# Kernel optimization log

Measured on AMD Instinct MI355X. Metric: run time of the kernel, lower is better.

## Reference

```python
import jax, jax.numpy as jnp
import numpy as np

N, E, G = 50000, 500000, 64
DIN, ED, H1, H2, HD, OUT = 128, 32, 256, 128, 64, 8


def setup_inputs() -> dict:
    key = jax.random.key(0)
    ks = jax.random.split(key, 20)
    g = lambda i, shape: (jax.random.normal(ks[i], shape, jnp.float32) * 0.05)
    return dict(
        node_attr=jax.random.normal(ks[0], (N, DIN), jnp.float32),
        edge_attr=jax.random.normal(ks[1], (E, ED), jnp.float32),
        edge_src=jax.random.randint(ks[2], (E,), 0, N, jnp.int32),
        edge_dst=jax.random.randint(ks[3], (E,), 0, N, jnp.int32),
        batch=jnp.sort(jax.random.randint(ks[4], (N,), 0, G, jnp.int32)),
        Wl1=g(5, (DIN, H1)), bl1=jnp.zeros((H1,), jnp.float32),
        Wr1=g(6, (DIN, H1)), br1=jnp.zeros((H1,), jnp.float32),
        We1=g(7, (ED, H1)), att1=g(8, (H1,)), b1=jnp.zeros((H1,), jnp.float32),
        Wl2=g(9, (H1, H2)), bl2=jnp.zeros((H2,), jnp.float32),
        Wr2=g(10, (H1, H2)), br2=jnp.zeros((H2,), jnp.float32),
        We2=g(11, (ED, H2)), att2=g(12, (H2,)), b2=jnp.zeros((H2,), jnp.float32),
        Wd1=g(13, (H2, HD)), bd1=jnp.zeros((HD,), jnp.float32),
        bn_gamma=jnp.ones((HD,), jnp.float32), bn_beta=jnp.zeros((HD,), jnp.float32),
        bn_mean=jnp.zeros((HD,), jnp.float32), bn_var=jnp.ones((HD,), jnp.float32),
        Wd2=g(14, (HD, OUT)), bd2=jnp.zeros((OUT,), jnp.float32),
    )


def gatv2(x, src, dst, eattr, Wl, bl, Wr, br, We, att, bias, n):
    # PyG GATv2Conv, heads=1: add self-loops (fill_value='mean' for edge_attr)
    ones = jnp.ones((eattr.shape[0],), x.dtype)
    deg = jax.ops.segment_sum(ones, dst, n)
    loop_attr = jax.ops.segment_sum(eattr, dst, n) / jnp.maximum(deg, 1.0)[:, None]
    loop = jnp.arange(n, dtype=src.dtype)
    src_ = jnp.concatenate([src, loop])
    dst_ = jnp.concatenate([dst, loop])
    eattr_ = jnp.concatenate([eattr, loop_attr], axis=0)
    xl = x @ Wl + bl  # [n, C] source transform (lin_l)
    xr = x @ Wr + br  # [n, C] dest transform (lin_r)
    # edge-wise GATv2 score: a^T LeakyReLU(xl_j + xr_i + We e_ij)
    e = jax.nn.leaky_relu(xl[src_] + xr[dst_] + eattr_ @ We, 0.2) @ att  # [E+n]
    m = jax.ops.segment_max(e, dst_, n)
    w = jnp.exp(e - m[dst_])
    denom = jax.ops.segment_sum(w, dst_, n)
    alpha = w / denom[dst_]
    return jax.ops.segment_sum(alpha[:, None] * xl[src_], dst_, n) + bias


def reference(node_attr, edge_attr, edge_src, edge_dst, batch,
              Wl1, bl1, Wr1, br1, We1, att1, b1,
              Wl2, bl2, Wr2, br2, We2, att2, b2,
              Wd1, bd1, bn_gamma, bn_beta, bn_mean, bn_var, Wd2, bd2):
    x = jax.nn.relu(gatv2(node_attr, edge_src, edge_dst, edge_attr,
                          Wl1, bl1, Wr1, br1, We1, att1, b1, N))
    x = jax.nn.relu(gatv2(x, edge_src, edge_dst, edge_attr,
                          Wl2, bl2, Wr2, br2, We2, att2, b2, N))
    # global mean pool over graphs
    cnt = jax.ops.segment_sum(jnp.ones((N,), x.dtype), batch, G)
    x = jax.ops.segment_sum(x, batch, G) / jnp.maximum(cnt, 1.0)[:, None]
    x = x @ Wd1 + bd1
    # BatchNorm1d in eval mode (running stats); dropout is identity in eval
    x = (x - bn_mean) / jnp.sqrt(bn_var + 1e-5) * bn_gamma + bn_beta
    x = jax.nn.leaky_relu(x, 0.1)
    return x @ Wd2 + bd2
```

## Files before the change

### kernel.cpp

```cpp
#include <hip/hip_runtime.h>
#include <cstdint>
#include <cstddef>
#include <cmath>

constexpr int Nn = 50000;
constexpr int Ne = 500000;
constexpr int Gg = 64;
constexpr int DIN = 128, ED = 32, H1 = 256, H2 = 128, HD = 64, NOUT = 8;

typedef __attribute__((ext_vector_type(8))) short bf16x8;
typedef __attribute__((ext_vector_type(4))) float f32x4;

__device__ __forceinline__ unsigned short f2bf(float x) {
    unsigned u = __float_as_uint(x);
    u += 0x7FFFu + ((u >> 16) & 1u);
    return (unsigned short)(u >> 16);
}
__device__ __forceinline__ float bf2f(unsigned short h) {
    return __uint_as_float(((unsigned)h) << 16);
}

__global__ void count_deg_kernel(const int* __restrict__ dst, int* __restrict__ deg) {
    int e = blockIdx.x * 256 + threadIdx.x;
    if (e < Ne) atomicAdd(&deg[dst[e]], 1);
}

__global__ __launch_bounds__(1024) void scan_kernel(const int* __restrict__ deg,
                                                    int* __restrict__ row_start) {
    __shared__ int part[1024];
    int t = threadIdx.x;
    const int chunk = (Nn + 1023) / 1024;
    int lo = t * chunk;
    int hi = min(lo + chunk, Nn);
    int s = 0;
    for (int i = lo; i < hi; i++) s += deg[i];
    part[t] = s;
    __syncthreads();
    for (int off = 1; off < 1024; off <<= 1) {
        int add = (t >= off) ? part[t - off] : 0;
        __syncthreads();
        part[t] += add;
        __syncthreads();
    }
    int base = (t == 0) ? 0 : part[t - 1];
    for (int i = lo; i < hi; i++) { row_start[i] = base; base += deg[i]; }
    if (t == 0) row_start[Nn] = Ne;
}

__global__ void scatter_kernel(const int* __restrict__ dst, const int* __restrict__ row_start,
                               int* __restrict__ cursor, int* __restrict__ perm) {
    int e = blockIdx.x * 256 + threadIdx.x;
    if (e < Ne) {
        int d = dst[e];
        int p = atomicAdd(&cursor[d], 1);
        perm[row_start[d] + p] = e;
    }
}

__global__ void build_sd_kernel(const int* __restrict__ perm, const int* __restrict__ src,
                                const int* __restrict__ dst,
                                int* __restrict__ srcv, int* __restrict__ dstv) {
    int j = blockIdx.x * 256 + threadIdx.x;
    if (j < Ne) {
        int e = perm[j];
        srcv[j] = src[e];
        dstv[j] = dst[e];
    }
}

__global__ void loop_attr_kernel(const int* __restrict__ row_start, const int* __restrict__ perm,
                                 const float* __restrict__ eattr, float* __restrict__ loop_attr) {
    int tid = blockIdx.x * 256 + threadIdx.x;
    if (tid >= Nn * 8) return;
    int i = tid >> 3, q = (tid & 7) << 2;
    int r0 = row_start[i], r1 = row_start[i + 1];
    float4 s = make_float4(0.f, 0.f, 0.f, 0.f);
    for (int j = r0; j < r1; j++) {
        int e = perm[j];
        float4 v = *(const float4*)(eattr + (size_t)e * ED + q);
        s.x += v.x; s.y += v.y; s.z += v.z; s.w += v.w;
    }
    float inv = 1.0f / fmaxf((float)(r1 - r0), 1.0f);
    *(float4*)(loop_attr + (size_t)i * ED + q) =
        make_float4(s.x * inv, s.y * inv, s.z * inv, s.w * inv);
}

__global__ void cvt_wt6_kernel(
    const float* __restrict__ We1, unsigned short* __restrict__ w1hi, unsigned short* __restrict__ w1lo,
    const float* __restrict__ We2, unsigned short* __restrict__ w2hi, unsigned short* __restrict__ w2lo,
    const float* __restrict__ Wl1, unsigned short* __restrict__ wl1hi, unsigned short* __restrict__ wl1lo,
    const float* __restrict__ Wr1, unsigned short* __restrict__ wr1hi, unsigned short* __restrict__ wr1lo,
    const float* __restrict__ Wl2, unsigned short* __restrict__ wl2hi, unsigned short* __restrict__ wl2lo,
    const float* __restrict__ Wr2, unsigned short* __restrict__ wr2hi, unsigned short* __restrict__ wr2lo) {
    const float* W; unsigned short *hi, *lo; int K, N;
    switch (blockIdx.y) {
        case 0: W = We1; hi = w1hi;  lo = w1lo;  K = ED;  N = H1; break;
        case 1: W = We2; hi = w2hi;  lo = w2lo;  K = ED;  N = H2; break;
        case 2: W = Wl1; hi = wl1hi; lo = wl1lo; K = DIN; N = H1; break;
        case 3: W = Wr1; hi = wr1hi; lo = wr1lo; K = DIN; N = H1; break;
        case 4: W = Wl2; hi = wl2hi; lo = wl2lo; K = H1;  N = H2; break;
        default: W = Wr2; hi = wr2hi; lo = wr2lo; K = H1;  N = H2; break;
    }
    int t = blockIdx.x * 256 + threadIdx.x;
    if (t >= K * N) return;
    int col = t / K, k = t % K;
    float x = W[(size_t)k * N + col];
    unsigned short h = f2bf(x);
    hi[t] = h;
    lo[t] = f2bf(x - bf2f(h));
}

template <int K, int N>
__global__ __launch_bounds__(256) void gemm_mfma_kernel(
    int M, const float* __restrict__ A,
    const unsigned short* __restrict__ wt0hi, const unsigned short* __restrict__ wt0lo,
    const float* __restrict__ bias0, float* __restrict__ C0,
    const unsigned short* __restrict__ wt1hi, const unsigned short* __restrict__ wt1lo,
    const float* __restrict__ bias1, float* __restrict__ C1) {
    const unsigned short* wthi = blockIdx.z ? wt1hi : wt0hi;
    const unsigned short* wtlo = blockIdx.z ? wt1lo : wt0lo;
    const float* bias = blockIdx.z ? bias1 : bias0;
    float* Cc = blockIdx.z ? C1 : C0;
    constexpr int KC = (K > 128) ? 128 : K;
    constexpr int P = KC + 8;
    constexpr int NT = N / 64;
    constexpr int CH = KC / 4;
    __shared__ unsigned short Ah[64 * P], Al[64 * P];
    const int tid = threadIdx.x;
    const int m0 = blockIdx.y * 64;

    const int wv = tid >> 6, lane = tid & 63;
    const int g = lane >> 4, li = lane & 15;
    const int nb = wv * (N / 4);

    f32x4 acc[4][NT];
#pragma unroll
    for (int n = 0; n < NT; n++) {
        float bc = bias[nb + n * 16 + li];
#pragma unroll
        for (int m = 0; m < 4; m++) {
            acc[m][n][0] = bc; acc[m][n][1] = bc; acc[m][n][2] = bc; acc[m][n][3] = bc;
        }
    }

    for (int kc = 0; kc < K; kc += KC) {
        for (int t = tid; t < 64 * CH; t += 256) {
            int row = t / CH, c = t % CH;
            int gr = min(m0 + row, M - 1);
            float4 v = *(const float4*)(A + (size_t)gr * K + kc + c * 4);
            unsigned short h0 = f2bf(v.x), h1 = f2bf(v.y), h2 = f2bf(v.z), h3 = f2bf(v.w);
            unsigned short l0 = f2bf(v.x - bf2f(h0)), l1 = f2bf(v.y - bf2f(h1));
            unsigned short l2 = f2bf(v.z - bf2f(h2)), l3 = f2bf(v.w - bf2f(h3));
            *(ushort4*)&Ah[row * P + c * 4] = make_ushort4(h0, h1, h2, h3);
            *(ushort4*)&Al[row * P + c * 4] = make_ushort4(l0, l1, l2, l3);
        }
        __syncthreads();

#pragma unroll
        for (int kt = 0; kt < KC / 32; kt++) {
            bf16x8 afh[4], afl[4], bfh[NT], bfl[NT];
#pragma unroll
            for (int m = 0; m < 4; m++) {
                afh[m] = *(const bf16x8*)&Ah[(m * 16 + li) * P + kt * 32 + g * 8];
                afl[m] = *(const bf16x8*)&Al[(m * 16 + li) * P + kt * 32 + g * 8];
            }
#pragma unroll
            for (int n = 0; n < NT; n++) {
                int col = nb + n * 16 + li;
                bfh[n] = *(const bf16x8*)(wthi + (size_t)col * K + kc + kt * 32 + g * 8);
                bfl[n] = *(const bf16x8*)(wtlo + (size_t)col * K + kc + kt * 32 + g * 8);
            }
#pragma unroll
            for (int m = 0; m < 4; m++)
#pragma unroll
                for (int n = 0; n < NT; n++) {
                    acc[m][n] = __builtin_amdgcn_mfma_f32_16x16x32_bf16(afh[m], bfh[n], acc[m][n], 0, 0, 0);
                    acc[m][n] = __builtin_amdgcn_mfma_f32_16x16x32_bf16(afh[m], bfl[n], acc[m][n], 0, 0, 0);
                    acc[m][n] = __builtin_amdgcn_mfma_f32_16x16x32_bf16(afl[m], bfh[n], acc[m][n], 0, 0, 0);
                }
        }
        __syncthreads();
    }

#pragma unroll
    for (int m = 0; m < 4; m++)
#pragma unroll
        for (int n = 0; n < NT; n++) {
            int col = nb + n * 16 + li;
#pragma unroll
            for (int r = 0; r < 4; r++) {
                int node = m0 + m * 16 + g * 4 + r;
                if (node < M) Cc[(size_t)node * N + col] = acc[m][n][r];
            }
        }
}

template <int C>
__global__ __launch_bounds__((C / 64) * 64) void score_mfma4_kernel(
    int ecount, int eblocks, const int* __restrict__ perm,
    const int* __restrict__ srcv, const int* __restrict__ dstv,
    const float* __restrict__ eattr, float* __restrict__ esc,
    int ncount, const float* __restrict__ lattr, float* __restrict__ nsc,
    const float* __restrict__ xl, const float* __restrict__ xr,
    const unsigned short* __restrict__ wthi, const unsigned short* __restrict__ wtlo,
    const float* __restrict__ att) {
    constexpr int WPB = C / 64;
    constexpr int NTHR = WPB * 64;
    __shared__ unsigned short Ah[64 * 40], Al[64 * 40];
    __shared__ float pw[WPB][64];
    const int tid = threadIdx.x;
    const bool selfp = (int)blockIdx.x >= eblocks;
    const int bid = selfp ? ((int)blockIdx.x - eblocks) : (int)blockIdx.x;
    const int count = selfp ? ncount : ecount;
    const float* attr = selfp ? lattr : eattr;
    float* sc_out = selfp ? nsc : esc;
    const int j0 = bid * 64;

    for (int t = tid; t < 64 * 8; t += NTHR) {
        int row = t >> 3, c = t & 7;
        int j = min(j0 + row, count - 1);
        int e = selfp ? j : perm[j];
        float4 v = *(const float4*)(attr + (size_t)e * ED + c * 4);
        unsigned short h0 = f2bf(v.x), h1 = f2bf(v.y), h2 = f2bf(v.z), h3 = f2bf(v.w);
        unsigned short l0 = f2bf(v.x - bf2f(h0)), l1 = f2bf(v.y - bf2f(h1));
        unsigned short l2 = f2bf(v.z - bf2f(h2)), l3 = f2bf(v.w - bf2f(h3));
        *(ushort4*)&Ah[row * 40 + c * 4] = make_ushort4(h0, h1, h2, h3);
        *(ushort4*)&Al[row * 40 + c * 4] = make_ushort4(l0, l1, l2, l3);
    }
    __syncthreads();

    const int wv = tid >> 6, lane = tid & 63;
    const int g = lane >> 4, li = lane & 15;
    const int cb = wv * 64 + g * 4;

    bf16x8 af_h[4], af_l[4];
#pragma unroll
    for (int m = 0; m < 4; m++) {
        int col = wv * 64 + m * 16 + li;
        af_h[m] = *(const bf16x8*)(wthi + (size_t)col * ED + g * 8);
        af_l[m] = *(const bf16x8*)(wtlo + (size_t)col * ED + g * 8);
    }
    float4 attv[4];
#pragma unroll
    for (int m = 0; m < 4; m++) attv[m] = *(const float4*)(att + cb + m * 16);

    int s0, d0, s1, d1, s2, d2, s3, d3;
    {
        int j;
        j = min(j0 + 0 * 16 + li, count - 1);
        s0 = selfp ? j : srcv[j]; d0 = selfp ? j : dstv[j];
        j = min(j0 + 1 * 16 + li, count - 1);
        s1 = selfp ? j : srcv[j]; d1 = selfp ? j : dstv[j];
        j = min(j0 + 2 * 16 + li, count - 1);
        s2 = selfp ? j : srcv[j]; d2 = selfp ? j : dstv[j];
        j = min(j0 + 3 * 16 + li, count - 1);
        s3 = selfp ? j : srcv[j]; d3 = selfp ? j : dstv[j];
    }

    auto pf = [&](int n, int sE, int dE, bf16x8& bh, bf16x8& bl,
                  float4 (&xlv)[4], float4 (&xrv)[4]) {
        bh = *(const bf16x8*)&Ah[(n * 16 + li) * 40 + g * 8];
        bl = *(const bf16x8*)&Al[(n * 16 + li) * 40 + g * 8];
        const float* pl = xl + (size_t)sE * C + cb;
        const float* pr = xr + (size_t)dE * C + cb;
#pragma unroll
        for (int m = 0; m < 4; m++) {
            xlv[m] = *(const float4*)(pl + m * 16);
            xrv[m] = *(const float4*)(pr + m * 16);
        }
    };
    auto comp = [&](int n, bf16x8 bh, bf16x8 bl,
                    const float4 (&xlv)[4], const float4 (&xrv)[4]) {
        f32x4 acc[4];
#pragma unroll
        for (int m = 0; m < 4; m++) {
            acc[m][0] = xlv[m].x + xrv[m].x; acc[m][1] = xlv[m].y + xrv[m].y;
            acc[m][2] = xlv[m].z + xrv[m].z; acc[m][3] = xlv[m].w + xrv[m].w;
        }
#pragma unroll
        for (int m = 0; m < 4; m++) {
            acc[m] = __builtin_amdgcn_mfma_f32_16x16x32_bf16(af_h[m], bh, acc[m], 0, 0, 0);
            acc[m] = __builtin_amdgcn_mfma_f32_16x16x32_bf16(af_h[m], bl, acc[m], 0, 0, 0);
            acc[m] = __builtin_amdgcn_mfma_f32_16x16x32_bf16(af_l[m], bh, acc[m], 0, 0, 0);
        }
        float s = 0.f;
#pragma unroll
        for (int m = 0; m < 4; m++) {
            const float av[4] = {attv[m].x, attv[m].y, attv[m].z, attv[m].w};
#pragma unroll
            for (int r = 0; r < 4; r++) {
                float z = acc[m][r];
                z = z > 0.f ? z : 0.2f * z;
                s = fmaf(z, av[r], s);
            }
        }
        s += __shfl_xor(s, 16);
        s += __shfl_xor(s, 32);
        if (lane < 16) pw[wv][n * 16 + li] = s;
    };

    bf16x8 bhA, blA, bhB, blB;
    float4 xlA[4], xrA[4], xlB[4], xrB[4];
    pf(0, s0, d0, bhA, blA, xlA, xrA);
    pf(1, s1, d1, bhB, blB, xlB, xrB);
    comp(0, bhA, blA, xlA, xrA);
    pf(2, s2, d2, bhA, blA, xlA, xrA);
    comp(1, bhB, blB, xlB, xrB);
    pf(3, s3, d3, bhB, blB, xlB, xrB);
    comp(2, bhA, blA, xlA, xrA);
    comp(3, bhB, blB, xlB, xrB);

    __syncthreads();
    if (tid < 64) {
        float s = pw[0][tid];
#pragma unroll
        for (int w = 1; w < WPB; w++) s += pw[w][tid];
        int j = j0 + tid;
        if (j < count) sc_out[j] = s;
    }
}

template <int C>
__global__ __launch_bounds__(256) void aggregate2_kernel(
    const int* __restrict__ row_start, const int* __restrict__ srcv,
    const float* __restrict__ scores, const float* __restrict__ sscore,
    const float* __restrict__ xl, const float* __restrict__ bias,
    float* __restrict__ xout) {
    constexpr int VP = C / 64;
    const int wave = threadIdx.x >> 6, lane = threadIdx.x & 63;
    const int i = blockIdx.x * 4 + wave;
    if (i >= Nn) return;
    const int r0 = row_start[i], r1 = row_start[i + 1];

    float mx = sscore[i];
    for (int j = r0 + lane; j < r1; j += 64) mx = fmaxf(mx, scores[j]);
#pragma unroll
    for (int off = 32; off >= 1; off >>= 1) mx = fmaxf(mx, __shfl_xor(mx, off));

    float l = 0.f;
    float acc[VP];
#pragma unroll
    for (int j = 0; j < VP; j++) acc[j] = 0.f;

    float wA[4], xA[4][VP];
    auto load_batch = [&](int j0, float* w, float (*x)[VP]) {
#pragma unroll
        for (int q = 0; q < 4; q++) {
            int j = min(j0 + q, r1 - 1);
            w[q] = scores[j];
            const float* p = xl + (size_t)srcv[j] * C + lane * VP;
            if constexpr (VP == 4) {
                float4 v = *(const float4*)p;
                x[q][0] = v.x; x[q][1] = v.y; x[q][2] = v.z; x[q][3] = v.w;
            } else {
                float2 v = *(const float2*)p;
                x[q][0] = v.x; x[q][1] = v.y;
            }
        }
    };
    if (r0 < r1) load_batch(r0, wA, xA);

    for (int j0 = r0; j0 < r1; j0 += 4) {
        float wB[4], xB[4][VP];
        if (j0 + 4 < r1) load_batch(j0 + 4, wB, xB);
        const int nb = min(4, r1 - j0);
        for (int q = 0; q < nb; q++) {
            float w = __expf(wA[q] - mx);
            l += w;
#pragma unroll
            for (int j = 0; j < VP; j++) acc[j] = fmaf(w, xA[q][j], acc[j]);
        }
        if (j0 + 4 < r1) {
#pragma unroll
            for (int q = 0; q < 4; q++) {
                wA[q] = wB[q];
#pragma unroll
                for (int j = 0; j < VP; j++) xA[q][j] = xB[q][j];
            }
        }
    }

    {
        float w = __expf(sscore[i] - mx);
        l += w;
        const float* p = xl + (size_t)i * C + lane * VP;
        if constexpr (VP == 4) {
            float4 v = *(const float4*)p;
            acc[0] = fmaf(w, v.x, acc[0]); acc[1] = fmaf(w, v.y, acc[1]);
            acc[2] = fmaf(w, v.z, acc[2]); acc[3] = fmaf(w, v.w, acc[3]);
        } else {
            float2 v = *(const float2*)p;
            acc[0] = fmaf(w, v.x, acc[0]); acc[1] = fmaf(w, v.y, acc[1]);
        }
    }

    float invl = 1.0f / l;
    float* xo = xout + (size_t)i * C + lane * VP;
    if constexpr (VP == 4) {
        float4 bv = *(const float4*)(bias + lane * 4);
        float4 o;
        o.x = fmaxf(fmaf(acc[0], invl, bv.x), 0.f);
        o.y = fmaxf(fmaf(acc[1], invl, bv.y), 0.f);
        o.z = fmaxf(fmaf(acc[2], invl, bv.z), 0.f);
        o.w = fmaxf(fmaf(acc[3], invl, bv.w), 0.f);
        *(float4*)xo = o;
    } else {
        float2 bv = *(const float2*)(bias + lane * 2);
        float2 o;
        o.x = fmaxf(fmaf(acc[0], invl, bv.x), 0.f);
        o.y = fmaxf(fmaf(acc[1], invl, bv.y), 0.f);
        *(float2*)xo = o;
    }
}

__global__ __launch_bounds__(128) void pool2_kernel(const float* __restrict__ x2,
                                                    const int* __restrict__ batch,
                                                    float* __restrict__ pooled,
                                                    float* __restrict__ cnt) {
    const int c = threadIdx.x;
    const int chunk = (Nn + gridDim.x - 1) / gridDim.x;
    int lo = blockIdx.x * chunk;
    int hi = min(lo + chunk, Nn);
    if (lo >= hi) return;
    int gcur = batch[lo];
    float acc = 0.f, ncnt = 0.f;
    for (int i = lo; i < hi; i++) {
        int g = batch[i];
        if (g != gcur) {
            atomicAdd(&pooled[gcur * H2 + c], acc);
            if (c == 0) atomicAdd(&cnt[gcur], ncnt);
            acc = 0.f; ncnt = 0.f; gcur = g;
        }
        acc += x2[(size_t)i * H2 + c];
        ncnt += 1.f;
    }
    atomicAdd(&pooled[gcur * H2 + c], acc);
    if (c == 0) atomicAdd(&cnt[gcur], ncnt);
}

__global__ __launch_bounds__(64) void head_kernel(
    const float* __restrict__ pooled, const float* __restrict__ cnt,
    const float* __restrict__ Wd1, const float* __restrict__ bd1,
    const float* __restrict__ gamma, const float* __restrict__ beta,
    const float* __restrict__ mean, const float* __restrict__ var,
    const float* __restrict__ Wd2, const float* __restrict__ bd2,
    float* __restrict__ out) {
    __shared__ float xm[H2];
    __shared__ float h[HD];
    int g = blockIdx.x, t = threadIdx.x;
    float c = fmaxf(cnt[g], 1.0f);
    for (int i = t; i < H2; i += 64) xm[i] = pooled[g * H2 + i] / c;
    __syncthreads();
    float a = bd1[t];
    for (int k = 0; k < H2; k++) a = fmaf(xm[k], Wd1[k * HD + t], a);
    a = (a - mean[t]) / sqrtf(var[t] + 1e-5f) * gamma[t] + beta[t];
    a = a > 0.f ? a : 0.1f * a;
    h[t] = a;
    __syncthreads();
    if (t < NOUT) {
        float o = bd2[t];
        for (int k = 0; k < HD; k++) o = fmaf(h[k], Wd2[k * NOUT + t], o);
        out[g * NOUT + t] = o;
    }
}

extern "C" void kernel_launch(void* const* d_in, const int* in_sizes, int n_in,
                              void* d_out, int out_size, void* d_ws, size_t ws_size,
                              hipStream_t stream) {
    const float* node_attr = (const float*)d_in[0];
    const float* edge_attr = (const float*)d_in[1];
    const int* edge_src = (const int*)d_in[2];
    const int* edge_dst = (const int*)d_in[3];
    const int* batch = (const int*)d_in[4];
    const float* Wl1 = (const float*)d_in[5];  const float* bl1 = (const float*)d_in[6];
    const float* Wr1 = (const float*)d_in[7];  const float* br1 = (const float*)d_in[8];
    const float* We1 = (const float*)d_in[9];  const float* att1 = (const float*)d_in[10];
    const float* b1 = (const float*)d_in[11];
    const float* Wl2 = (const float*)d_in[12]; const float* bl2 = (const float*)d_in[13];
    const float* Wr2 = (const float*)d_in[14]; const float* br2 = (const float*)d_in[15];
    const float* We2 = (const float*)d_in[16]; const float* att2 = (const float*)d_in[17];
    const float* b2 = (const float*)d_in[18];
    const float* Wd1 = (const float*)d_in[19]; const float* bd1 = (const float*)d_in[20];
    const float* bn_gamma = (const float*)d_in[21]; const float* bn_beta = (const float*)d_in[22];
    const float* bn_mean = (const float*)d_in[23];  const float* bn_var = (const float*)d_in[24];
    const float* Wd2 = (const float*)d_in[25]; const float* bd2 = (const float*)d_in[26];
    float* out = (float*)d_out;

    char* ws = (char*)d_ws;
    size_t off = 0;
    auto alloc = [&](size_t bytes) -> char* {
        char* p = ws + off;
        off = (off + bytes + 255) & ~(size_t)255;
        return p;
    };
    int* deg         = (int*)alloc((size_t)Nn * 4);
    int* row_start   = (int*)alloc((size_t)(Nn + 1) * 4);
    int* cursor      = (int*)alloc((size_t)Nn * 4);
    int* perm        = (int*)alloc((size_t)Ne * 4);
    int* srcv        = (int*)alloc((size_t)Ne * 4);
    int* dstv        = (int*)alloc((size_t)Ne * 4);
    float* loop_attr = (float*)alloc((size_t)Nn * ED * 4);
    float* scores    = (float*)alloc((size_t)Ne * 4);
    float* sscore    = (float*)alloc((size_t)Nn * 4);
    float* pooled    = (float*)alloc((size_t)Gg * H2 * 4);
    float* cnt       = (float*)alloc((size_t)Gg * 4);
    float* xlb       = (float*)alloc((size_t)Nn * H1 * 4);
    float* xrb       = (float*)alloc((size_t)Nn * H1 * 4);
    float* x1        = (float*)alloc((size_t)Nn * H1 * 4);
    unsigned short* w1hi = (unsigned short*)alloc((size_t)H1 * ED * 2);
    unsigned short* w1lo = (unsigned short*)alloc((size_t)H1 * ED * 2);
    unsigned short* w2hi = (unsigned short*)alloc((size_t)H2 * ED * 2);
    unsigned short* w2lo = (unsigned short*)alloc((size_t)H2 * ED * 2);
    unsigned short* wl1hi = (unsigned short*)alloc((size_t)H1 * DIN * 2);
    unsigned short* wl1lo = (unsigned short*)alloc((size_t)H1 * DIN * 2);
    unsigned short* wr1hi = (unsigned short*)alloc((size_t)H1 * DIN * 2);
    unsigned short* wr1lo = (unsigned short*)alloc((size_t)H1 * DIN * 2);
    unsigned short* wl2hi = (unsigned short*)alloc((size_t)H2 * H1 * 2);
    unsigned short* wl2lo = (unsigned short*)alloc((size_t)H2 * H1 * 2);
    unsigned short* wr2hi = (unsigned short*)alloc((size_t)H2 * H1 * 2);
    unsigned short* wr2lo = (unsigned short*)alloc((size_t)H2 * H1 * 2);

    hipMemsetAsync(deg, 0, (size_t)Nn * 4, stream);
    hipMemsetAsync(cursor, 0, (size_t)Nn * 4, stream);
    hipMemsetAsync(pooled, 0, (size_t)Gg * H2 * 4, stream);
    hipMemsetAsync(cnt, 0, (size_t)Gg * 4, stream);

    count_deg_kernel<<<(Ne + 255) / 256, 256, 0, stream>>>(edge_dst, deg);
    scan_kernel<<<1, 1024, 0, stream>>>(deg, row_start);
    scatter_kernel<<<(Ne + 255) / 256, 256, 0, stream>>>(edge_dst, row_start, cursor, perm);
    build_sd_kernel<<<(Ne + 255) / 256, 256, 0, stream>>>(perm, edge_src, edge_dst, srcv, dstv);
    loop_attr_kernel<<<(Nn * 8 + 255) / 256, 256, 0, stream>>>(row_start, perm, edge_attr, loop_attr);

    cvt_wt6_kernel<<<dim3((DIN * H1 + 255) / 256, 6), 256, 0, stream>>>(
        We1, w1hi, w1lo, We2, w2hi, w2lo, Wl1, wl1hi, wl1lo,
        Wr1, wr1hi, wr1lo, Wl2, wl2hi, wl2lo, Wr2, wr2hi, wr2lo);

    const int eb64 = (Ne + 63) / 64, nb64 = (Nn + 63) / 64;
    const int gb = (Nn + 63) / 64;

    gemm_mfma_kernel<DIN, H1><<<dim3(1, gb, 2), 256, 0, stream>>>(
        Nn, node_attr, wl1hi, wl1lo, bl1, xlb, wr1hi, wr1lo, br1, xrb);
    score_mfma4_kernel<H1><<<eb64 + nb64, 256, 0, stream>>>(
        Ne, eb64, perm, srcv, dstv, edge_attr, scores,
        Nn, loop_attr, sscore, xlb, xrb, w1hi, w1lo, att1);
    aggregate2_kernel<H1><<<(Nn + 3) / 4, 256, 0, stream>>>(
        row_start, srcv, scores, sscore, xlb, b1, x1);

    gemm_mfma_kernel<H1, H2><<<dim3(1, gb, 2), 256, 0, stream>>>(
        Nn, x1, wl2hi, wl2lo, bl2, xlb, wr2hi, wr2lo, br2, xrb);
    score_mfma4_kernel<H2><<<eb64 + nb64, 128, 0, stream>>>(
        Ne, eb64, perm, srcv, dstv, edge_attr, scores,
        Nn, loop_attr, sscore, xlb, xrb, w2hi, w2lo, att2);
    float* x2 = x1;
    aggregate2_kernel<H2><<<(Nn + 3) / 4, 256, 0, stream>>>(
        row_start, srcv, scores, sscore, xlb, b2, x2);

    pool2_kernel<<<256, 128, 0, stream>>>(x2, batch, pooled, cnt);
    head_kernel<<<Gg, 64, 0, stream>>>(pooled, cnt, Wd1, bd1, bn_gamma, bn_beta,
                                       bn_mean, bn_var, Wd2, bd2, out);
}
```

Baseline: 782.6 us.

## Stage gathered xl+xr rows in shared memory with coalesced loads in score kernel

```diff
diff --git a/kernel.cpp b/kernel.cpp
--- a/kernel.cpp
+++ b/kernel.cpp
@@ -196,7 +196,7 @@
 }
 
 template <int C>
-__global__ __launch_bounds__((C / 64) * 64) void score_mfma4_kernel(
+__global__ __launch_bounds__((C / 64) * 64) void score_mfma5_kernel(
     int ecount, int eblocks, const int* __restrict__ perm,
     const int* __restrict__ srcv, const int* __restrict__ dstv,
     const float* __restrict__ eattr, float* __restrict__ esc,
@@ -206,17 +206,21 @@
     const float* __restrict__ att) {
     constexpr int WPB = C / 64;
     constexpr int NTHR = WPB * 64;
-    __shared__ unsigned short Ah[64 * 40], Al[64 * 40];
-    __shared__ float pw[WPB][64];
+    constexpr int EB = 32;
+    constexpr int XP = C + 4;
+    constexpr int TPR = C / 4;
+    __shared__ float xs[EB * XP];
+    __shared__ unsigned short Ah[EB * 40], Al[EB * 40];
+    __shared__ float pw[WPB][EB];
     const int tid = threadIdx.x;
     const bool selfp = (int)blockIdx.x >= eblocks;
     const int bid = selfp ? ((int)blockIdx.x - eblocks) : (int)blockIdx.x;
     const int count = selfp ? ncount : ecount;
     const float* attr = selfp ? lattr : eattr;
     float* sc_out = selfp ? nsc : esc;
-    const int j0 = bid * 64;
-
-    for (int t = tid; t < 64 * 8; t += NTHR) {
+    const int j0 = bid * EB;
+
+    for (int t = tid; t < EB * 8; t += NTHR) {
         int row = t >> 3, c = t & 7;
         int j = min(j0 + row, count - 1);
         int e = selfp ? j : perm[j];
@@ -227,6 +231,16 @@
         *(ushort4*)&Ah[row * 40 + c * 4] = make_ushort4(h0, h1, h2, h3);
         *(ushort4*)&Al[row * 40 + c * 4] = make_ushort4(l0, l1, l2, l3);
     }
+    for (int u = tid; u < EB * TPR; u += NTHR) {
+        int row = u / TPR, c4 = u % TPR;
+        int j = min(j0 + row, count - 1);
+        int s, d;
+        if (selfp) { s = j; d = j; } else { s = srcv[j]; d = dstv[j]; }
+        float4 a = *(const float4*)(xl + (size_t)s * C + c4 * 4);
+        float4 b = *(const float4*)(xr + (size_t)d * C + c4 * 4);
+        *(float4*)&xs[row * XP + c4 * 4] =
+            make_float4(a.x + b.x, a.y + b.y, a.z + b.z, a.w + b.w);
+    }
     __syncthreads();
 
     const int wv = tid >> 6, lane = tid & 63;
@@ -244,38 +258,15 @@
 #pragma unroll
     for (int m = 0; m < 4; m++) attv[m] = *(const float4*)(att + cb + m * 16);
 
-    int s0, d0, s1, d1, s2, d2, s3, d3;
-    {
-        int j;
-        j = min(j0 + 0 * 16 + li, count - 1);
-        s0 = selfp ? j : srcv[j]; d0 = selfp ? j : dstv[j];
-        j = min(j0 + 1 * 16 + li, count - 1);
-        s1 = selfp ? j : srcv[j]; d1 = selfp ? j : dstv[j];
-        j = min(j0 + 2 * 16 + li, count - 1);
-        s2 = selfp ? j : srcv[j]; d2 = selfp ? j : dstv[j];
-        j = min(j0 + 3 * 16 + li, count - 1);
-        s3 = selfp ? j : srcv[j]; d3 = selfp ? j : dstv[j];
-    }
-
-    auto pf = [&](int n, int sE, int dE, bf16x8& bh, bf16x8& bl,
-                  float4 (&xlv)[4], float4 (&xrv)[4]) {
-        bh = *(const bf16x8*)&Ah[(n * 16 + li) * 40 + g * 8];
-        bl = *(const bf16x8*)&Al[(n * 16 + li) * 40 + g * 8];
-        const float* pl = xl + (size_t)sE * C + cb;
-        const float* pr = xr + (size_t)dE * C + cb;
+#pragma unroll
+    for (int n = 0; n < EB / 16; n++) {
+        bf16x8 bh = *(const bf16x8*)&Ah[(n * 16 + li) * 40 + g * 8];
+        bf16x8 bl = *(const bf16x8*)&Al[(n * 16 + li) * 40 + g * 8];
+        f32x4 acc[4];
 #pragma unroll
         for (int m = 0; m < 4; m++) {
-            xlv[m] = *(const float4*)(pl + m * 16);
-            xrv[m] = *(const float4*)(pr + m * 16);
-        }
-    };
-    auto comp = [&](int n, bf16x8 bh, bf16x8 bl,
-                    const float4 (&xlv)[4], const float4 (&xrv)[4]) {
-        f32x4 acc[4];
-#pragma unroll
-        for (int m = 0; m < 4; m++) {
-            acc[m][0] = xlv[m].x + xrv[m].x; acc[m][1] = xlv[m].y + xrv[m].y;
-            acc[m][2] = xlv[m].z + xrv[m].z; acc[m][3] = xlv[m].w + xrv[m].w;
+            float4 v = *(const float4*)&xs[(n * 16 + li) * XP + cb + m * 16];
+            acc[m][0] = v.x; acc[m][1] = v.y; acc[m][2] = v.z; acc[m][3] = v.w;
         }
 #pragma unroll
         for (int m = 0; m < 4; m++) {
@@ -297,21 +288,10 @@
         s += __shfl_xor(s, 16);
         s += __shfl_xor(s, 32);
         if (lane < 16) pw[wv][n * 16 + li] = s;
-    };
-
-    bf16x8 bhA, blA, bhB, blB;
-    float4 xlA[4], xrA[4], xlB[4], xrB[4];
-    pf(0, s0, d0, bhA, blA, xlA, xrA);
-    pf(1, s1, d1, bhB, blB, xlB, xrB);
-    comp(0, bhA, blA, xlA, xrA);
-    pf(2, s2, d2, bhA, blA, xlA, xrA);
-    comp(1, bhB, blB, xlB, xrB);
-    pf(3, s3, d3, bhB, blB, xlB, xrB);
-    comp(2, bhA, blA, xlA, xrA);
-    comp(3, bhB, blB, xlB, xrB);
+    }
 
     __syncthreads();
-    if (tid < 64) {
+    if (tid < EB) {
         float s = pw[0][tid];
 #pragma unroll
         for (int w = 1; w < WPB; w++) s += pw[w][tid];
@@ -535,21 +515,21 @@
         We1, w1hi, w1lo, We2, w2hi, w2lo, Wl1, wl1hi, wl1lo,
         Wr1, wr1hi, wr1lo, Wl2, wl2hi, wl2lo, Wr2, wr2hi, wr2lo);
 
-    const int eb64 = (Ne + 63) / 64, nb64 = (Nn + 63) / 64;
+    const int eb32 = (Ne + 31) / 32, nb32 = (Nn + 31) / 32;
     const int gb = (Nn + 63) / 64;
 
     gemm_mfma_kernel<DIN, H1><<<dim3(1, gb, 2), 256, 0, stream>>>(
         Nn, node_attr, wl1hi, wl1lo, bl1, xlb, wr1hi, wr1lo, br1, xrb);
-    score_mfma4_kernel<H1><<<eb64 + nb64, 256, 0, stream>>>(
-        Ne, eb64, perm, srcv, dstv, edge_attr, scores,
+    score_mfma5_kernel<H1><<<eb32 + nb32, 256, 0, stream>>>(
+        Ne, eb32, perm, srcv, dstv, edge_attr, scores,
         Nn, loop_attr, sscore, xlb, xrb, w1hi, w1lo, att1);
     aggregate2_kernel<H1><<<(Nn + 3) / 4, 256, 0, stream>>>(
         row_start, srcv, scores, sscore, xlb, b1, x1);
 
     gemm_mfma_kernel<H1, H2><<<dim3(1, gb, 2), 256, 0, stream>>>(
         Nn, x1, wl2hi, wl2lo, bl2, xlb, wr2hi, wr2lo, br2, xrb);
-    score_mfma4_kernel<H2><<<eb64 + nb64, 128, 0, stream>>>(
-        Ne, eb64, perm, srcv, dstv, edge_attr, scores,
+    score_mfma5_kernel<H2><<<eb32 + nb32, 128, 0, stream>>>(
+        Ne, eb32, perm, srcv, dstv, edge_attr, scores,
         Nn, loop_attr, sscore, xlb, xrb, w2hi, w2lo, att2);
     float* x2 = x1;
     aggregate2_kernel<H2><<<(Nn + 3) / 4, 256, 0, stream>>>(
```

Result: slower. 847.0 us (+8.2%).
